# Kernel optimization log

Measured on AMD Instinct MI355X. Metric: run time of the kernel, lower is better.

The kernel has to match this reference:

```python
import jax, jax.numpy as jnp
import numpy as np


def setup_inputs() -> dict:
    key = jax.random.key(0)
    ks = jax.random.split(key, 10)
    B, D_X, D_H, D_S, D_T = 16384, 256, 512, 128, 128
    G = 4 * D_H
    sc = lambda d: 1.0 / np.sqrt(d)
    return {
        "x": jax.random.normal(ks[0], (B, D_X), jnp.float32),
        "h": jax.random.normal(ks[1], (B, D_H), jnp.float32),
        "c": jax.random.normal(ks[2], (B, D_H), jnp.float32),
        "spatial_per_step": jax.random.normal(ks[3], (B, D_S), jnp.float32),
        "temporal_per_step": jax.random.normal(ks[4], (B, D_T), jnp.float32),
        "W_x": jax.random.normal(ks[5], (D_X, G), jnp.float32) * sc(D_X),
        "W_h": jax.random.normal(ks[6], (D_H, G), jnp.float32) * sc(D_H),
        "b_h": jax.random.normal(ks[7], (G,), jnp.float32) * 0.01,
        "W_s": jax.random.normal(ks[8], (D_S, G), jnp.float32) * sc(D_S),
        "W_t": jax.random.normal(ks[9], (D_T, G), jnp.float32) * sc(D_T),
    }


def reference(x, h, c, spatial_per_step, temporal_per_step, W_x, W_h, b_h, W_s, W_t):
    H = W_h.shape[0]  # hidden_size
    # Four gate projections summed (the fusion opportunity): [B, 4H]
    preact = (x @ W_x) + (h @ W_h + b_h) + (spatial_per_step @ W_s) + (temporal_per_step @ W_t)
    i_g = jax.nn.sigmoid(preact[:, 0 * H:1 * H])
    f_g = jax.nn.sigmoid(preact[:, 1 * H:2 * H])
    o_g = jax.nn.sigmoid(preact[:, 2 * H:3 * H])
    c_g = jnp.tanh(preact[:, 3 * H:4 * H])
    c_new = f_g * c + i_g * c_g
    # NOTE: faithful to the source, h = tanh(o * c) (not o * tanh(c))
    h_new = jnp.tanh(o_g * c_new)
    return (h_new, c_new)
```

## Files before the change

kernel.cpp:

```cpp
#include <hip/hip_runtime.h>
#include <hip/hip_bf16.h>
#include <cstdint>

#define B_DIM 16384
#define DX 256
#define DH 512
#define DS 128
#define DT 128
#define KDIM 1024
#define NDIM 2048
#define HOUT 512

typedef __attribute__((ext_vector_type(8))) short short8;
typedef __attribute__((ext_vector_type(4))) float floatx4;

union bf16x8 {
  short8 v;
  __hip_bfloat16 b[8];
};

__device__ __forceinline__ float fast_sigmoid(float x) {
  return 1.f / (1.f + __expf(-x));
}
__device__ __forceinline__ float fast_tanh(float x) {
  float e = __expf(-2.f * x);
  return (1.f - e) / (1.f + e);
}


__global__ __launch_bounds__(256) void pack_A(
    const float* __restrict__ x, const float* __restrict__ h,
    const float* __restrict__ s, const float* __restrict__ t,
    __hip_bfloat16* __restrict__ Ap) {
  int tid = blockIdx.x * 256 + threadIdx.x;
  int i = tid & 63;
  int tt = (tid >> 6) & 15;
  int tile = tid >> 10;
  int kb = tile & 15, mb = tile >> 4;
  int sp = tt >> 3, c = tt & 7;
  int b = mb * 128 + c * 16 + (i >> 2);
  int k = kb * 64 + sp * 32 + (i & 3) * 8;
  const float* p;
  if (k < 256)      p = x + (size_t)b * DX + k;
  else if (k < 768) p = h + (size_t)b * DH + (k - 256);
  else if (k < 896) p = s + (size_t)b * DS + (k - 768);
  else              p = t + (size_t)b * DT + (k - 896);
  floatx4 v0 = *(const floatx4*)p;
  floatx4 v1 = *(const floatx4*)(p + 4);
  bf16x8 o;
#pragma unroll
  for (int j = 0; j < 4; ++j) {
    o.b[j]     = __float2bfloat16(v0[j]);
    o.b[4 + j] = __float2bfloat16(v1[j]);
  }
  *(short8*)(Ap + (size_t)tid * 8) = o.v;
}

__global__ __launch_bounds__(256) void pack_W(
    const float* __restrict__ Wx, const float* __restrict__ Wh,
    const float* __restrict__ Ws, const float* __restrict__ Wt,
    __hip_bfloat16* __restrict__ Wp) {
  int tid = blockIdx.x * 256 + threadIdx.x;
  int i = tid & 63;
  int tt = (tid >> 6) & 15;
  int tile = tid >> 10;
  int kb = tile & 15, nblk = tile >> 4;
  int sp = tt >> 3, c = tt & 7;
  int nl = c * 16 + (i >> 2);
  int k = kb * 64 + sp * 32 + (i & 3) * 8;
  int wn = nl >> 6, g = (nl >> 4) & 3, hl = nl & 15;
  int col = g * 512 + nblk * 32 + wn * 16 + hl;
  const float* src; int kl;
  if (k < 256)      { src = Wx; kl = k; }
  else if (k < 768) { src = Wh; kl = k - 256; }
  else if (k < 896) { src = Ws; kl = k - 768; }
  else              { src = Wt; kl = k - 896; }
  bf16x8 o;
#pragma unroll
  for (int r = 0; r < 8; ++r)
    o.b[r] = __float2bfloat16(src[(size_t)(kl + r) * NDIM + col]);
  *(short8*)(Wp + (size_t)tid * 8) = o.v;
}

__global__ __launch_bounds__(256, 4) void lstm_gemm(
    const __hip_bfloat16* __restrict__ Ap, const __hip_bfloat16* __restrict__ Wp,
    const float* __restrict__ bh, const float* __restrict__ c_in,
    float* __restrict__ out) {
  __shared__ unsigned short As[128 * 32];
  __shared__ unsigned short Bs[128 * 32];

  const int tid = threadIdx.x;
  const int lane = tid & 63;
  const int wid = tid >> 6;
  const int wm = wid & 1;
  const int wn = wid >> 1;
  const int q = lane >> 4;
  const int fr = lane & 15;
  const int mb = blockIdx.y;
  const int nblk = blockIdx.x;
  const int m0 = mb * 128;

  floatx4 acc[4][4];
#pragma unroll
  for (int i = 0; i < 4; ++i)
#pragma unroll
    for (int j = 0; j < 4; ++j) acc[i][j] = (floatx4)0.f;

  for (int p = 0; p < 32; ++p) {
    const size_t abase = ((size_t)((mb * 16 + (p >> 1)) * 16 + (p & 1) * 8)) * 512;
    const size_t bbase = ((size_t)((nblk * 16 + (p >> 1)) * 16 + (p & 1) * 8)) * 512;
#pragma unroll
    for (int j = 0; j < 2; ++j) {
      const int chunk = wid * 2 + j;
      __builtin_amdgcn_global_load_lds(
          (const __attribute__((address_space(1))) void*)
              (Ap + abase + (size_t)chunk * 512 + lane * 8),
          (__attribute__((address_space(3))) void*)&As[chunk * 512], 16, 0, 0);
      __builtin_amdgcn_global_load_lds(
          (const __attribute__((address_space(1))) void*)
              (Wp + bbase + (size_t)chunk * 512 + lane * 8),
          (__attribute__((address_space(3))) void*)&Bs[chunk * 512], 16, 0, 0);
    }
    __syncthreads();

    short8 af[4], bf[4];
#pragma unroll
    for (int i = 0; i < 4; ++i) {
      af[i] = *(const short8*)&As[(wm * 64 + i * 16 + fr) * 32 + q * 8];
      bf[i] = *(const short8*)&Bs[(wn * 64 + i * 16 + fr) * 32 + q * 8];
    }
#pragma unroll
    for (int mi = 0; mi < 4; ++mi)
#pragma unroll
      for (int ni = 0; ni < 4; ++ni)
        acc[mi][ni] = __builtin_amdgcn_mfma_f32_16x16x32_bf16(
            af[mi], bf[ni], acc[mi][ni], 0, 0, 0);
    __syncthreads();
  }

  const int hh = nblk * 32 + wn * 16 + fr;
  float bias[4];
#pragma unroll
  for (int g = 0; g < 4; ++g) bias[g] = bh[g * 512 + hh];

#pragma unroll
  for (int mi = 0; mi < 4; ++mi) {
#pragma unroll
    for (int r = 0; r < 4; ++r) {
      const size_t grow = (size_t)(m0 + wm * 64 + mi * 16 + q * 4 + r);
      const float pi = acc[mi][0][r] + bias[0];
      const float pf = acc[mi][1][r] + bias[1];
      const float po = acc[mi][2][r] + bias[2];
      const float pc = acc[mi][3][r] + bias[3];
      const float ig = fast_sigmoid(pi);
      const float fg = fast_sigmoid(pf);
      const float og = fast_sigmoid(po);
      const float cg = fast_tanh(pc);
      const float cc = fg * c_in[grow * HOUT + hh] + ig * cg;
      out[grow * HOUT + hh] = fast_tanh(og * cc);
      out[(size_t)B_DIM * HOUT + grow * HOUT + hh] = cc;
    }
  }
}

extern "C" void kernel_launch(void* const* d_in, const int* in_sizes, int n_in,
                              void* d_out, int out_size, void* d_ws, size_t ws_size,
                              hipStream_t stream) {
  const float* x  = (const float*)d_in[0];
  const float* h  = (const float*)d_in[1];
  const float* c  = (const float*)d_in[2];
  const float* sp = (const float*)d_in[3];
  const float* tp = (const float*)d_in[4];
  const float* Wx = (const float*)d_in[5];
  const float* Wh = (const float*)d_in[6];
  const float* bh = (const float*)d_in[7];
  const float* Ws = (const float*)d_in[8];
  const float* Wt = (const float*)d_in[9];
  float* out = (float*)d_out;

  __hip_bfloat16* Ap = (__hip_bfloat16*)d_ws;
  __hip_bfloat16* Wp = (__hip_bfloat16*)((char*)d_ws + (size_t)B_DIM * KDIM * 2);

  pack_A<<<dim3(B_DIM * KDIM / 8 / 256), dim3(256), 0, stream>>>(x, h, sp, tp, Ap);
  pack_W<<<dim3(NDIM * KDIM / 8 / 256), dim3(256), 0, stream>>>(Wx, Wh, Ws, Wt, Wp);
  lstm_gemm<<<dim3(NDIM / 128, B_DIM / 128), dim3(256), 0, stream>>>(Ap, Wp, bh, c, out);
}
```

Baseline: 242.6 us.

## Double-buffer LDS tiles in LSTM GEMM and merge pack kernels into one launch

The GEMM main loop now keeps two LDS buffers for each of the A and W tiles. It issues the async global-to-LDS loads for the next K-step right after the barrier, so those loads overlap the MFMA work on the current step, and one of the two barriers per iteration is dropped. The separate A and W packing kernels are combined into a single launch that picks the packing role by block index, saving one kernel launch. LDS use per block doubles to 32KB, which could limit occupancy against the 4-blocks-per-CU launch bound.

After: 247.9 us. +2.2%, slower.

```diff
diff --git a/kernel.cpp b/kernel.cpp
--- a/kernel.cpp
+++ b/kernel.cpp
@@ -28,66 +28,68 @@
 }
 
 
-__global__ __launch_bounds__(256) void pack_A(
+#define PACKA_BLOCKS (B_DIM * KDIM / 8 / 256)
+#define PACKW_BLOCKS (NDIM * KDIM / 8 / 256)
+
+__global__ __launch_bounds__(256) void pack_AW(
     const float* __restrict__ x, const float* __restrict__ h,
     const float* __restrict__ s, const float* __restrict__ t,
-    __hip_bfloat16* __restrict__ Ap) {
-  int tid = blockIdx.x * 256 + threadIdx.x;
-  int i = tid & 63;
-  int tt = (tid >> 6) & 15;
-  int tile = tid >> 10;
-  int kb = tile & 15, mb = tile >> 4;
-  int sp = tt >> 3, c = tt & 7;
-  int b = mb * 128 + c * 16 + (i >> 2);
-  int k = kb * 64 + sp * 32 + (i & 3) * 8;
-  const float* p;
-  if (k < 256)      p = x + (size_t)b * DX + k;
-  else if (k < 768) p = h + (size_t)b * DH + (k - 256);
-  else if (k < 896) p = s + (size_t)b * DS + (k - 768);
-  else              p = t + (size_t)b * DT + (k - 896);
-  floatx4 v0 = *(const floatx4*)p;
-  floatx4 v1 = *(const floatx4*)(p + 4);
-  bf16x8 o;
-#pragma unroll
-  for (int j = 0; j < 4; ++j) {
-    o.b[j]     = __float2bfloat16(v0[j]);
-    o.b[4 + j] = __float2bfloat16(v1[j]);
-  }
-  *(short8*)(Ap + (size_t)tid * 8) = o.v;
-}
-
-__global__ __launch_bounds__(256) void pack_W(
     const float* __restrict__ Wx, const float* __restrict__ Wh,
     const float* __restrict__ Ws, const float* __restrict__ Wt,
-    __hip_bfloat16* __restrict__ Wp) {
-  int tid = blockIdx.x * 256 + threadIdx.x;
-  int i = tid & 63;
-  int tt = (tid >> 6) & 15;
-  int tile = tid >> 10;
-  int kb = tile & 15, nblk = tile >> 4;
-  int sp = tt >> 3, c = tt & 7;
-  int nl = c * 16 + (i >> 2);
-  int k = kb * 64 + sp * 32 + (i & 3) * 8;
-  int wn = nl >> 6, g = (nl >> 4) & 3, hl = nl & 15;
-  int col = g * 512 + nblk * 32 + wn * 16 + hl;
-  const float* src; int kl;
-  if (k < 256)      { src = Wx; kl = k; }
-  else if (k < 768) { src = Wh; kl = k - 256; }
-  else if (k < 896) { src = Ws; kl = k - 768; }
-  else              { src = Wt; kl = k - 896; }
-  bf16x8 o;
-#pragma unroll
-  for (int r = 0; r < 8; ++r)
-    o.b[r] = __float2bfloat16(src[(size_t)(kl + r) * NDIM + col]);
-  *(short8*)(Wp + (size_t)tid * 8) = o.v;
+    __hip_bfloat16* __restrict__ Ap, __hip_bfloat16* __restrict__ Wp) {
+  if (blockIdx.x < PACKA_BLOCKS) {
+    int tid = blockIdx.x * 256 + threadIdx.x;
+    int i = tid & 63;
+    int tt = (tid >> 6) & 15;
+    int tile = tid >> 10;
+    int kb = tile & 15, mb = tile >> 4;
+    int sp = tt >> 3, c = tt & 7;
+    int b = mb * 128 + c * 16 + (i >> 2);
+    int k = kb * 64 + sp * 32 + (i & 3) * 8;
+    const float* p;
+    if (k < 256)      p = x + (size_t)b * DX + k;
+    else if (k < 768) p = h + (size_t)b * DH + (k - 256);
+    else if (k < 896) p = s + (size_t)b * DS + (k - 768);
+    else              p = t + (size_t)b * DT + (k - 896);
+    floatx4 v0 = *(const floatx4*)p;
+    floatx4 v1 = *(const floatx4*)(p + 4);
+    bf16x8 o;
+#pragma unroll
+    for (int j = 0; j < 4; ++j) {
+      o.b[j]     = __float2bfloat16(v0[j]);
+      o.b[4 + j] = __float2bfloat16(v1[j]);
+    }
+    *(short8*)(Ap + (size_t)tid * 8) = o.v;
+  } else {
+    int tid = (blockIdx.x - PACKA_BLOCKS) * 256 + threadIdx.x;
+    int i = tid & 63;
+    int tt = (tid >> 6) & 15;
+    int tile = tid >> 10;
+    int kb = tile & 15, nblk = tile >> 4;
+    int sp = tt >> 3, c = tt & 7;
+    int nl = c * 16 + (i >> 2);
+    int k = kb * 64 + sp * 32 + (i & 3) * 8;
+    int wn = nl >> 6, g = (nl >> 4) & 3, hl = nl & 15;
+    int col = g * 512 + nblk * 32 + wn * 16 + hl;
+    const float* src; int kl;
+    if (k < 256)      { src = Wx; kl = k; }
+    else if (k < 768) { src = Wh; kl = k - 256; }
+    else if (k < 896) { src = Ws; kl = k - 768; }
+    else              { src = Wt; kl = k - 896; }
+    bf16x8 o;
+#pragma unroll
+    for (int r = 0; r < 8; ++r)
+      o.b[r] = __float2bfloat16(src[(size_t)(kl + r) * NDIM + col]);
+    *(short8*)(Wp + (size_t)tid * 8) = o.v;
+  }
 }
 
 __global__ __launch_bounds__(256, 4) void lstm_gemm(
     const __hip_bfloat16* __restrict__ Ap, const __hip_bfloat16* __restrict__ Wp,
     const float* __restrict__ bh, const float* __restrict__ c_in,
     float* __restrict__ out) {
-  __shared__ unsigned short As[128 * 32];
-  __shared__ unsigned short Bs[128 * 32];
+  __shared__ unsigned short As[2][128 * 32];
+  __shared__ unsigned short Bs[2][128 * 32];
 
   const int tid = threadIdx.x;
   const int lane = tid & 63;
@@ -106,28 +108,42 @@
 #pragma unroll
     for (int j = 0; j < 4; ++j) acc[i][j] = (floatx4)0.f;
 
-  for (int p = 0; p < 32; ++p) {
-    const size_t abase = ((size_t)((mb * 16 + (p >> 1)) * 16 + (p & 1) * 8)) * 512;
-    const size_t bbase = ((size_t)((nblk * 16 + (p >> 1)) * 16 + (p & 1) * 8)) * 512;
+  const int c0 = wid * 2;
+  const size_t lanoff = (size_t)lane * 8;
+
+  auto issue = [&](int p) {
+    const size_t abase =
+        ((size_t)((mb * 16 + (p >> 1)) * 16 + (p & 1) * 8)) * 512;
+    const size_t bbase =
+        ((size_t)((nblk * 16 + (p >> 1)) * 16 + (p & 1) * 8)) * 512;
+    const int buf = p & 1;
 #pragma unroll
     for (int j = 0; j < 2; ++j) {
-      const int chunk = wid * 2 + j;
+      const int chunk = c0 + j;
       __builtin_amdgcn_global_load_lds(
           (const __attribute__((address_space(1))) void*)
-              (Ap + abase + (size_t)chunk * 512 + lane * 8),
-          (__attribute__((address_space(3))) void*)&As[chunk * 512], 16, 0, 0);
+              (Ap + abase + (size_t)chunk * 512 + lanoff),
+          (__attribute__((address_space(3))) void*)&As[buf][chunk * 512],
+          16, 0, 0);
       __builtin_amdgcn_global_load_lds(
           (const __attribute__((address_space(1))) void*)
-              (Wp + bbase + (size_t)chunk * 512 + lane * 8),
-          (__attribute__((address_space(3))) void*)&Bs[chunk * 512], 16, 0, 0);
-    }
+              (Wp + bbase + (size_t)chunk * 512 + lanoff),
+          (__attribute__((address_space(3))) void*)&Bs[buf][chunk * 512],
+          16, 0, 0);
+    }
+  };
+
+  issue(0);
+  for (int p = 0; p < 32; ++p) {
     __syncthreads();
-
+    if (p + 1 < 32) issue(p + 1);
+
+    const int buf = p & 1;
     short8 af[4], bf[4];
 #pragma unroll
     for (int i = 0; i < 4; ++i) {
-      af[i] = *(const short8*)&As[(wm * 64 + i * 16 + fr) * 32 + q * 8];
-      bf[i] = *(const short8*)&Bs[(wn * 64 + i * 16 + fr) * 32 + q * 8];
+      af[i] = *(const short8*)&As[buf][(wm * 64 + i * 16 + fr) * 32 + q * 8];
+      bf[i] = *(const short8*)&Bs[buf][(wn * 64 + i * 16 + fr) * 32 + q * 8];
     }
 #pragma unroll
     for (int mi = 0; mi < 4; ++mi)
@@ -135,7 +151,6 @@
       for (int ni = 0; ni < 4; ++ni)
         acc[mi][ni] = __builtin_amdgcn_mfma_f32_16x16x32_bf16(
             af[mi], bf[ni], acc[mi][ni], 0, 0, 0);
-    __syncthreads();
   }
 
   const int hh = nblk * 32 + wn * 16 + fr;
@@ -181,7 +196,7 @@
   __hip_bfloat16* Ap = (__hip_bfloat16*)d_ws;
   __hip_bfloat16* Wp = (__hip_bfloat16*)((char*)d_ws + (size_t)B_DIM * KDIM * 2);
 
-  pack_A<<<dim3(B_DIM * KDIM / 8 / 256), dim3(256), 0, stream>>>(x, h, sp, tp, Ap);
-  pack_W<<<dim3(NDIM * KDIM / 8 / 256), dim3(256), 0, stream>>>(Wx, Wh, Ws, Wt, Wp);
+  pack_AW<<<dim3(PACKA_BLOCKS + PACKW_BLOCKS), dim3(256), 0, stream>>>(
+      x, h, sp, tp, Wx, Wh, Ws, Wt, Ap, Wp);
   lstm_gemm<<<dim3(NDIM / 128, B_DIM / 128), dim3(256), 0, stream>>>(Ap, Wp, bh, c, out);
 }
```
